# Performance work log

Measured on AMD Instinct MI355X. Metric: run time of the kernel, lower is better.

Reference implementation:

```python
import jax, jax.numpy as jnp
import numpy as np

# Module configuration (from init_kwargs)
N, C_IN, C_OUT, L, V, P = 4, 64, 64, 1024, 25, 3
KERNEL_SIZE, STRIDE = 9, 1
EPS = 1e-5


def _toeplitz(length):
    # Faithful to: sum_i pad(eye(L - stride*i), (i*stride, 0, 0, i*stride))
    # -> ones at [r, r + i*stride] for i in range(kernel_size // stride)
    t = jnp.zeros((length, length), dtype=jnp.float32)
    for i in range(KERNEL_SIZE // STRIDE):  # small fixed loop over taps
        t = t + jnp.eye(length, k=i * STRIDE, dtype=jnp.float32)
    return t


def setup_inputs() -> dict:
    key = jax.random.key(0)
    k0, k1, k2, k3 = jax.random.split(key, 4)
    x = jax.random.normal(k0, (N, C_IN, L, V), dtype=jnp.float32)
    A = jax.random.uniform(k1, (P, V, V), dtype=jnp.float32)
    edge_importance = jnp.ones((P, V, V), dtype=jnp.float32)
    conv_w = jax.random.normal(k2, (C_OUT * P, C_IN, 1, 1), dtype=jnp.float32) * 0.05
    conv_b = jax.random.normal(k3, (C_OUT * P,), dtype=jnp.float32) * 0.05
    gamma = jnp.ones((C_OUT,), dtype=jnp.float32)
    beta = jnp.zeros((C_OUT,), dtype=jnp.float32)
    return {"x": x, "A": A, "edge_importance": edge_importance,
            "conv_w": conv_w, "conv_b": conv_b, "gamma": gamma, "beta": beta}


def reference(x, A, edge_importance, conv_w, conv_b, gamma, beta):
    n, _, l, v = x.shape
    res = x  # residual: in_channels == out_channels and stride == 1 -> identity

    # 1x1 conv: (N, C_in, L, V) -> (N, P*C_out, L, V)
    w = conv_w[:, :, 0, 0]  # (P*C_out, C_in)
    y = jnp.einsum('nclv,kc->nklv', x, w) + conv_b[None, :, None, None]

    # split into P chunks of C_out along channels, stack, permute -> (N, L, P, C_out, V)
    y = y.reshape(n, P, C_OUT, l, v).transpose(0, 3, 1, 2, 4)

    # partition-wise graph adjacency matmul with edge-importance mask
    y = jnp.einsum('nlpcv,pvw->nlpcw', y, A * edge_importance)

    # Toeplitz temporal conv: (N, P, C, V, L) @ (L, L)
    y = y.transpose(0, 2, 3, 4, 1)
    y = jnp.matmul(y, _toeplitz(l))
    y = y.sum(axis=1)            # sum over partitions -> (N, C, V, L)
    y = y.transpose(0, 1, 3, 2)  # (N, C, L, V)

    # BatchNorm2d with batch statistics (track_running_stats=False) + ReLU
    mean = y.mean(axis=(0, 2, 3), keepdims=True)
    var = y.var(axis=(0, 2, 3), keepdims=True)  # biased, as torch uses for normalization
    y = (y - mean) * jax.lax.rsqrt(var + EPS)
    y = y * gamma[None, :, None, None] + beta[None, :, None, None]
    y = jax.nn.relu(y)

    # do = Sequential(ReLU, Dropout(0.0)) applied to (y + res)
    return jax.nn.relu(y + res)
```

## Files before the change

### kernel.cpp

```cpp
#include <hip/hip_runtime.h>


typedef unsigned short ushort_t;
typedef __attribute__((ext_vector_type(8))) short short8;
typedef __attribute__((ext_vector_type(4))) float f32x4;
typedef __attribute__((ext_vector_type(4))) unsigned short us4;
typedef __attribute__((ext_vector_type(8))) unsigned short us8;

#define N_  4
#define CI_ 64
#define CO_ 64
#define L_  1024
#define V_  25
#define P_  3
#define KS_ 9
#define NLV 102400.0f
#define NREP 128

__device__ __forceinline__ float b2f(ushort_t u) {
  union { float f; unsigned int i; } c; c.i = ((unsigned int)u) << 16; return c.f;
}
__device__ __forceinline__ ushort_t f2b(float f) {
  union { float f; unsigned int i; } c; c.f = f;
  unsigned int u = c.i;
  u += 0x7fffu + ((u >> 16) & 1u);
  return (ushort_t)(u >> 16);
}

__global__ __launch_bounds__(256) void kwin(
    const float* __restrict__ x, ushort_t* __restrict__ xs,
    const float* __restrict__ A, const float* __restrict__ E,
    const float* __restrict__ cb, const float* __restrict__ W,
    ushort_t* __restrict__ a2raw, float* __restrict__ biastab,
    ushort_t* __restrict__ wb, float* __restrict__ statsbuf)
{
  const int chunk = blockIdx.x;
  const int n = blockIdx.y;
  const int tid = threadIdx.x;

  if (chunk == 128) {
    if (n != 0) return;
    __shared__ float colA[P_ * 32];
    if (tid < P_ * 32) {
      int p = tid >> 5, w = tid & 31;
      float s = 0.f;
      if (w < V_)
        for (int v = 0; v < V_; ++v) {
          int idx = (p * V_ + v) * V_ + w;
          s += A[idx] * E[idx];
        }
      colA[tid] = s;
    }
    for (int e = tid; e < 32 * 96; e += 256) {
      int w = e / 96, k = e - w * 96;
      int p = k >> 5, v = k & 31;
      float val = 0.f;
      if (w < V_ && v < V_) {
        int idx = (p * V_ + v) * V_ + w;
        val = A[idx] * E[idx];
      }
      a2raw[e] = f2b(val);
    }
    for (int e = tid; e < 192 * 64; e += 256) wb[e] = f2b(W[e]);
    __syncthreads();
    for (int e = tid; e < 32 * 64; e += 256) {
      int w = e >> 6, c = e & 63;
      float s = 0.f;
      for (int p = 0; p < P_; ++p) s += cb[p * 64 + c] * colA[p * 32 + w];
      biastab[e] = s;
    }
    for (int e = tid; e < NREP * 128; e += 256) statsbuf[e] = 0.f;
    return;
  }

  __shared__ ushort_t tile[64 * 402];
  const int l0 = chunk * 8;
  const long xn = (long)n * CI_ * L_ * V_;
  for (int m = tid; m < 6400; m += 256) {
    int ci = m / 100;
    int j4 = (m - ci * 100) * 4;
    f32x4 d;
    if (chunk == 0 && j4 < 200) {
      d = (f32x4){0.f, 0.f, 0.f, 0.f};
    } else {
      d = *(const f32x4*)(x + xn + (long)ci * (L_ * V_) + (l0 - 8) * V_ + j4);
    }
    ushort_t* dst = &tile[ci * 402 + j4];
    dst[0] = f2b(d[0]); dst[1] = f2b(d[1]); dst[2] = f2b(d[2]); dst[3] = f2b(d[3]);
  }
  __syncthreads();
  const long xsbase = ((long)n * L_ + l0) * 1600;
  for (int cid = tid; cid < 1600; cid += 256) {
    const int v = cid >> 6, ci = cid & 63;
    const ushort_t* col = &tile[ci * 402 + v];
    float s = 0.f;
#pragma unroll
    for (int li = 0; li < 9; ++li) s += b2f(col[li * 25]);
    xs[xsbase + cid] = f2b(s);
#pragma unroll
    for (int l_ = 1; l_ < 8; ++l_) {
      s += b2f(col[(l_ + 8) * 25]) - b2f(col[(l_ - 1) * 25]);
      xs[xsbase + l_ * 1600 + cid] = f2b(s);
    }
  }
}

__global__ __launch_bounds__(256, 4) void kmain(
    const ushort_t* __restrict__ xs,
    const ushort_t* __restrict__ Wb,
    const ushort_t* __restrict__ a2,
    const float*    __restrict__ biastab,
    ushort_t*       __restrict__ zb,
    float*          __restrict__ statsbuf)
{
  const int lb = blockIdx.x;
  const int n  = blockIdx.y;
  const int tid = threadIdx.x, lane = tid & 63, wv = tid >> 6;
  const int m16 = lane & 15, quad = lane >> 4;

  __shared__ __align__(16) ushort_t T1[13312];

  short8 af[3][2];
#pragma unroll
  for (int i = 0; i < 3; ++i) {
    const ushort_t* wrow = Wb + ((wv * 3 + i) * 16 + m16) * 64 + quad * 8;
    af[i][0] = *(const short8*)(wrow);
    af[i][1] = *(const short8*)(wrow + 32);
  }

  const ushort_t* xsb = xs + ((long)n * L_ + 4 * lb) * 1600;
  const int cbase = wv * 16 + quad * 4;
  float s1[4] = {0.f, 0.f, 0.f, 0.f}, s2[4] = {0.f, 0.f, 0.f, 0.f};

#pragma unroll
  for (int pair = 0; pair < 2; ++pair) {
    short8 bfr[4][2];
#pragma unroll
    for (int nt = 0; nt < 4; ++nt) {
      const int v = (nt & 1) * 16 + m16;
      const int l_ = pair * 2 + (nt >> 1);
#pragma unroll
      for (int ks = 0; ks < 2; ++ks) {
        short8 t = (short8){0, 0, 0, 0, 0, 0, 0, 0};
        if (v < V_)
          t = *(const short8*)(xsb + l_ * 1600 + v * 64 + ks * 32 + quad * 8);
        bfr[nt][ks] = t;
      }
    }

    f32x4 acc1[3][4];
#pragma unroll
    for (int i = 0; i < 3; ++i)
#pragma unroll
      for (int j = 0; j < 4; ++j) acc1[i][j] = (f32x4){0.f, 0.f, 0.f, 0.f};

#pragma unroll
    for (int i = 0; i < 3; ++i)
#pragma unroll
      for (int nt = 0; nt < 4; ++nt) {
        acc1[i][nt] = __builtin_amdgcn_mfma_f32_16x16x32_bf16(af[i][0], bfr[nt][0], acc1[i][nt], 0, 0, 0);
        acc1[i][nt] = __builtin_amdgcn_mfma_f32_16x16x32_bf16(af[i][1], bfr[nt][1], acc1[i][nt], 0, 0, 0);
      }

    if (pair) __syncthreads();
#pragma unroll
    for (int i = 0; i < 3; ++i) {
      const int mt = wv * 3 + i;
#pragma unroll
      for (int nt = 0; nt < 4; ++nt) {
        const int l_ = nt >> 1;
        const int col = (nt & 1) * 16 + m16;
#pragma unroll
        for (int r = 0; r < 4; ++r) {
          int k = mt * 16 + quad * 4 + r;
          T1[l_ * 6656 + (k & 63) * 104 + (k >> 6) * 32 + col] = f2b(acc1[i][nt][r]);
        }
      }
    }
    __syncthreads();

    short8 bfr2[2][3];
#pragma unroll
    for (int nt = 0; nt < 2; ++nt)
#pragma unroll
      for (int ks = 0; ks < 3; ++ks)
        bfr2[nt][ks] = *(const short8*)(a2 + (nt * 16 + m16) * 96 + ks * 32 + quad * 8);

    f32x4 acc2[2][2];
#pragma unroll
    for (int l_ = 0; l_ < 2; ++l_)
#pragma unroll
      for (int nt = 0; nt < 2; ++nt) acc2[l_][nt] = (f32x4){0.f, 0.f, 0.f, 0.f};

#pragma unroll
    for (int l_ = 0; l_ < 2; ++l_)
#pragma unroll
      for (int ks = 0; ks < 3; ++ks) {
        short8 afT = *(const short8*)(&T1[l_ * 6656 + (wv * 16 + m16) * 104 + ks * 32 + quad * 8]);
        acc2[l_][0] = __builtin_amdgcn_mfma_f32_16x16x32_bf16(afT, bfr2[0][ks], acc2[l_][0], 0, 0, 0);
        acc2[l_][1] = __builtin_amdgcn_mfma_f32_16x16x32_bf16(afT, bfr2[1][ks], acc2[l_][1], 0, 0, 0);
      }

#pragma unroll
    for (int l_ = 0; l_ < 2; ++l_) {
      const int l = 4 * lb + pair * 2 + l_;
      const float cnt = (float)(l + 1 < KS_ ? l + 1 : KS_);
#pragma unroll
      for (int nt = 0; nt < 2; ++nt) {
        const int w = nt * 16 + m16;
        if (w < V_) {
          f32x4 bias = *(const f32x4*)(biastab + w * 64 + cbase);
          us4 pack;
#pragma unroll
          for (int r = 0; r < 4; ++r) {
            pack[r] = f2b(acc2[l_][nt][r] + cnt * bias[r]);
            float zr = b2f(pack[r]);
            s1[r] += zr; s2[r] += zr * zr;
          }
          *(us4*)(&zb[(((long)(n * L_ + l) * V_ + w) << 6) + cbase]) = pack;
        }
      }
    }
  }
#pragma unroll
  for (int off = 1; off < 16; off <<= 1) {
#pragma unroll
    for (int r = 0; r < 4; ++r) {
      s1[r] += __shfl_xor(s1[r], off, 64);
      s2[r] += __shfl_xor(s2[r], off, 64);
    }
  }
  if (m16 == 0) {
    float* sb = statsbuf + ((n * 256 + lb) & (NREP - 1)) * 128;
#pragma unroll
    for (int r = 0; r < 4; ++r) {
      atomicAdd(&sb[cbase + r], s1[r]);
      atomicAdd(&sb[64 + cbase + r], s2[r]);
    }
  }
}

__global__ __launch_bounds__(256) void kapply(
    const ushort_t* __restrict__ zb, const float* __restrict__ x,
    const float* __restrict__ statsbuf,
    const float* __restrict__ gamma, const float* __restrict__ beta,
    float* __restrict__ out)
{
  const int n = blockIdx.y, chunk = blockIdx.x;
  const int tid = threadIdx.x;
  __shared__ ushort_t zl[200 * 66];
  __shared__ float red[4][64][2];
  __shared__ float sc[64], sh[64];
  const long zbase = (long)((n * L_ + chunk * 8) * V_) * 64;
  for (int m = tid; m < 6400; m += 256) {
    *(unsigned int*)(&zl[(m >> 5) * 66 + (m & 31) * 2]) =
        ((const unsigned int*)(zb + zbase))[m];
  }
  {
    const int c = tid & 63, grp = tid >> 6;
    float a = 0.f, b = 0.f;
    for (int k = grp; k < NREP; k += 4) {
      a += statsbuf[k * 128 + c];
      b += statsbuf[k * 128 + 64 + c];
    }
    red[grp][c][0] = a;
    red[grp][c][1] = b;
  }
  __syncthreads();
  if (tid < 64) {
    const float inv = 1.0f / NLV;
    float s  = red[0][tid][0] + red[1][tid][0] + red[2][tid][0] + red[3][tid][0];
    float sq = red[0][tid][1] + red[1][tid][1] + red[2][tid][1] + red[3][tid][1];
    float mean = s * inv;
    float var  = sq * inv - mean * mean;
    float rstd = rsqrtf(var + 1e-5f);
    float g = gamma[tid];
    sc[tid] = rstd * g;
    sh[tid] = beta[tid] - mean * rstd * g;
  }
  __syncthreads();
  const long obase = ((long)(n * 64) * L_ + chunk * 8) * V_;
  for (int m = tid; m < 3200; m += 256) {
    int c = m / 50, q = m - c * 50, rr = q * 4;
    long xi = obase + (long)c * (L_ * V_) + rr;
    f32x4 xv = *(const f32x4*)(x + xi);
    f32x4 o;
#pragma unroll
    for (int j = 0; j < 4; ++j) {
      float z = b2f(zl[(rr + j) * 66 + c]);
      float y = fmaxf(z * sc[c] + sh[c], 0.f);
      o[j] = fmaxf(y + xv[j], 0.f);
    }
    *(f32x4*)(out + xi) = o;
  }
}

extern "C" void kernel_launch(void* const* d_in, const int* in_sizes, int n_in,
                              void* d_out, int out_size, void* d_ws, size_t ws_size,
                              hipStream_t stream)
{
  const float* x     = (const float*)d_in[0];
  const float* A     = (const float*)d_in[1];
  const float* E     = (const float*)d_in[2];
  const float* W     = (const float*)d_in[3];
  const float* cb    = (const float*)d_in[4];
  const float* gamma = (const float*)d_in[5];
  const float* beta  = (const float*)d_in[6];
  float* out = (float*)d_out;

  char* ws = (char*)d_ws;
  const size_t XS_OFF   = 0;
  const size_t ZB_OFF   = 13107200;
  const size_t WB_OFF   = 26214400;
  const size_t A2_OFF   = WB_OFF + 32768;
  const size_t BIAS_OFF = A2_OFF + 16384;
  const size_t STAT_OFF = BIAS_OFF + 16384;
  ushort_t* xs       = (ushort_t*)(ws + XS_OFF);
  ushort_t* zb       = (ushort_t*)(ws + ZB_OFF);
  ushort_t* wb       = (ushort_t*)(ws + WB_OFF);
  ushort_t* a2       = (ushort_t*)(ws + A2_OFF);
  float*    biastab  = (float*)(ws + BIAS_OFF);
  float*    statsbuf = (float*)(ws + STAT_OFF);

  kwin  <<<dim3(129, N_), 256, 0, stream>>>(x, xs, A, E, cb, W, a2, biastab, wb,
                                            statsbuf);
  kmain <<<dim3(256, N_), 256, 0, stream>>>(xs, wb, a2, biastab, zb, statsbuf);
  kapply<<<dim3(128, N_), 256, 0, stream>>>(zb, x, statsbuf, gamma, beta, out);
}
```

Measured before the change: 135.1 us.

## Pack LDS writes, hoist kmain loads, swizzle apply tile, vectorize stats reduce

Several independent changes across three kernels. In kwin the bf16 tile writes are packed into 32-bit stores with a padded stride, and each thread now handles two channels so its xs stores are 32-bit. In kmain all xs B-fragment loads for both pairs are issued up front, and the MFMA accumulators are reduced to one row-tile at a time. In kapply the LDS transpose tile uses an XOR swizzle to cut bank conflicts, and the stats reduction reads float4. These trade extra register pressure in kmain for more overlap of load latency.

```diff
diff --git a/kernel.cpp b/kernel.cpp
--- a/kernel.cpp
+++ b/kernel.cpp
@@ -5,7 +5,6 @@
 typedef __attribute__((ext_vector_type(8))) short short8;
 typedef __attribute__((ext_vector_type(4))) float f32x4;
 typedef __attribute__((ext_vector_type(4))) unsigned short us4;
-typedef __attribute__((ext_vector_type(8))) unsigned short us8;
 
 #define N_  4
 #define CI_ 64
@@ -16,6 +15,7 @@
 #define KS_ 9
 #define NLV 102400.0f
 #define NREP 128
+#define TSTR 406
 
 __device__ __forceinline__ float b2f(ushort_t u) {
   union { float f; unsigned int i; } c; c.i = ((unsigned int)u) << 16; return c.f;
@@ -73,7 +73,7 @@
     return;
   }
 
-  __shared__ ushort_t tile[64 * 402];
+  __shared__ __align__(16) ushort_t tile[64 * TSTR];
   const int l0 = chunk * 8;
   const long xn = (long)n * CI_ * L_ * V_;
   for (int m = tid; m < 6400; m += 256) {
@@ -85,22 +85,28 @@
     } else {
       d = *(const f32x4*)(x + xn + (long)ci * (L_ * V_) + (l0 - 8) * V_ + j4);
     }
-    ushort_t* dst = &tile[ci * 402 + j4];
-    dst[0] = f2b(d[0]); dst[1] = f2b(d[1]); dst[2] = f2b(d[2]); dst[3] = f2b(d[3]);
+    unsigned int p0 = (unsigned int)f2b(d[0]) | ((unsigned int)f2b(d[1]) << 16);
+    unsigned int p1 = (unsigned int)f2b(d[2]) | ((unsigned int)f2b(d[3]) << 16);
+    *(unsigned int*)(&tile[ci * TSTR + j4])     = p0;
+    *(unsigned int*)(&tile[ci * TSTR + j4 + 2]) = p1;
   }
   __syncthreads();
   const long xsbase = ((long)n * L_ + l0) * 1600;
-  for (int cid = tid; cid < 1600; cid += 256) {
-    const int v = cid >> 6, ci = cid & 63;
-    const ushort_t* col = &tile[ci * 402 + v];
-    float s = 0.f;
-#pragma unroll
-    for (int li = 0; li < 9; ++li) s += b2f(col[li * 25]);
-    xs[xsbase + cid] = f2b(s);
+  for (int cp = tid; cp < 800; cp += 256) {
+    const int v = cp >> 5, ci = (cp & 31) * 2;
+    const ushort_t* c0 = &tile[ci * TSTR + v];
+    const ushort_t* c1 = c0 + TSTR;
+    float s0 = 0.f, s1 = 0.f;
+#pragma unroll
+    for (int li = 0; li < 9; ++li) { s0 += b2f(c0[li * 25]); s1 += b2f(c1[li * 25]); }
+    *(unsigned int*)(xs + xsbase + v * 64 + ci) =
+        (unsigned int)f2b(s0) | ((unsigned int)f2b(s1) << 16);
 #pragma unroll
     for (int l_ = 1; l_ < 8; ++l_) {
-      s += b2f(col[(l_ + 8) * 25]) - b2f(col[(l_ - 1) * 25]);
-      xs[xsbase + l_ * 1600 + cid] = f2b(s);
+      s0 += b2f(c0[(l_ + 8) * 25]) - b2f(c0[(l_ - 1) * 25]);
+      s1 += b2f(c1[(l_ + 8) * 25]) - b2f(c1[(l_ - 1) * 25]);
+      *(unsigned int*)(xs + xsbase + l_ * 1600 + v * 64 + ci) =
+          (unsigned int)f2b(s0) | ((unsigned int)f2b(s1) << 16);
     }
   }
 }
@@ -120,6 +126,24 @@
 
   __shared__ __align__(16) ushort_t T1[13312];
 
+  const ushort_t* xsb = xs + ((long)n * L_ + 4 * lb) * 1600;
+
+  short8 bfr[2][4][2];
+#pragma unroll
+  for (int pair = 0; pair < 2; ++pair)
+#pragma unroll
+    for (int nt = 0; nt < 4; ++nt) {
+      const int v = (nt & 1) * 16 + m16;
+      const int l_ = pair * 2 + (nt >> 1);
+#pragma unroll
+      for (int ks = 0; ks < 2; ++ks) {
+        short8 t = (short8){0, 0, 0, 0, 0, 0, 0, 0};
+        if (v < V_)
+          t = *(const short8*)(xsb + l_ * 1600 + v * 64 + ks * 32 + quad * 8);
+        bfr[pair][nt][ks] = t;
+      }
+    }
+
   short8 af[3][2];
 #pragma unroll
   for (int i = 0; i < 3; ++i) {
@@ -128,43 +152,23 @@
     af[i][1] = *(const short8*)(wrow + 32);
   }
 
-  const ushort_t* xsb = xs + ((long)n * L_ + 4 * lb) * 1600;
   const int cbase = wv * 16 + quad * 4;
   float s1[4] = {0.f, 0.f, 0.f, 0.f}, s2[4] = {0.f, 0.f, 0.f, 0.f};
 
 #pragma unroll
   for (int pair = 0; pair < 2; ++pair) {
-    short8 bfr[4][2];
-#pragma unroll
-    for (int nt = 0; nt < 4; ++nt) {
-      const int v = (nt & 1) * 16 + m16;
-      const int l_ = pair * 2 + (nt >> 1);
-#pragma unroll
-      for (int ks = 0; ks < 2; ++ks) {
-        short8 t = (short8){0, 0, 0, 0, 0, 0, 0, 0};
-        if (v < V_)
-          t = *(const short8*)(xsb + l_ * 1600 + v * 64 + ks * 32 + quad * 8);
-        bfr[nt][ks] = t;
-      }
-    }
-
-    f32x4 acc1[3][4];
-#pragma unroll
-    for (int i = 0; i < 3; ++i)
-#pragma unroll
-      for (int j = 0; j < 4; ++j) acc1[i][j] = (f32x4){0.f, 0.f, 0.f, 0.f};
-
-#pragma unroll
-    for (int i = 0; i < 3; ++i)
+    if (pair) __syncthreads();
+
+#pragma unroll
+    for (int i = 0; i < 3; ++i) {
+      f32x4 acc[4];
+#pragma unroll
+      for (int nt = 0; nt < 4; ++nt) acc[nt] = (f32x4){0.f, 0.f, 0.f, 0.f};
 #pragma unroll
       for (int nt = 0; nt < 4; ++nt) {
-        acc1[i][nt] = __builtin_amdgcn_mfma_f32_16x16x32_bf16(af[i][0], bfr[nt][0], acc1[i][nt], 0, 0, 0);
-        acc1[i][nt] = __builtin_amdgcn_mfma_f32_16x16x32_bf16(af[i][1], bfr[nt][1], acc1[i][nt], 0, 0, 0);
-      }
-
-    if (pair) __syncthreads();
-#pragma unroll
-    for (int i = 0; i < 3; ++i) {
+        acc[nt] = __builtin_amdgcn_mfma_f32_16x16x32_bf16(af[i][0], bfr[pair][nt][0], acc[nt], 0, 0, 0);
+        acc[nt] = __builtin_amdgcn_mfma_f32_16x16x32_bf16(af[i][1], bfr[pair][nt][1], acc[nt], 0, 0, 0);
+      }
       const int mt = wv * 3 + i;
 #pragma unroll
       for (int nt = 0; nt < 4; ++nt) {
@@ -173,7 +177,7 @@
 #pragma unroll
         for (int r = 0; r < 4; ++r) {
           int k = mt * 16 + quad * 4 + r;
-          T1[l_ * 6656 + (k & 63) * 104 + (k >> 6) * 32 + col] = f2b(acc1[i][nt][r]);
+          T1[l_ * 6656 + (k & 63) * 104 + (k >> 6) * 32 + col] = f2b(acc[nt][r]);
         }
       }
     }
@@ -248,29 +252,34 @@
 {
   const int n = blockIdx.y, chunk = blockIdx.x;
   const int tid = threadIdx.x;
-  __shared__ ushort_t zl[200 * 66];
-  __shared__ float red[4][64][2];
+  __shared__ __align__(16) ushort_t zl[200 * 66];
+  __shared__ f32x4 red[8][32];
   __shared__ float sc[64], sh[64];
   const long zbase = (long)((n * L_ + chunk * 8) * V_) * 64;
   for (int m = tid; m < 6400; m += 256) {
-    *(unsigned int*)(&zl[(m >> 5) * 66 + (m & 31) * 2]) =
-        ((const unsigned int*)(zb + zbase))[m];
+    const int row = m >> 5, c2 = (m & 31) * 2;
+    const int cs = c2 ^ (((row >> 2) & 31) << 1);
+    *(unsigned int*)(&zl[row * 66 + cs]) = ((const unsigned int*)(zb + zbase))[m];
   }
   {
-    const int c = tid & 63, grp = tid >> 6;
-    float a = 0.f, b = 0.f;
-    for (int k = grp; k < NREP; k += 4) {
-      a += statsbuf[k * 128 + c];
-      b += statsbuf[k * 128 + 64 + c];
-    }
-    red[grp][c][0] = a;
-    red[grp][c][1] = b;
+    const int s4 = tid & 31, grp = tid >> 5;
+    const f32x4* sb4 = (const f32x4*)statsbuf;
+    f32x4 a = (f32x4){0.f, 0.f, 0.f, 0.f};
+    for (int k = grp; k < NREP; k += 8) {
+      f32x4 v = sb4[k * 32 + s4];
+      a[0] += v[0]; a[1] += v[1]; a[2] += v[2]; a[3] += v[3];
+    }
+    red[grp][s4] = a;
   }
   __syncthreads();
   if (tid < 64) {
     const float inv = 1.0f / NLV;
-    float s  = red[0][tid][0] + red[1][tid][0] + red[2][tid][0] + red[3][tid][0];
-    float sq = red[0][tid][1] + red[1][tid][1] + red[2][tid][1] + red[3][tid][1];
+    float s = 0.f, sq = 0.f;
+#pragma unroll
+    for (int g = 0; g < 8; ++g) {
+      s  += red[g][tid >> 2][tid & 3];
+      sq += red[g][16 + (tid >> 2)][tid & 3];
+    }
     float mean = s * inv;
     float var  = sq * inv - mean * mean;
     float rstd = rsqrtf(var + 1e-5f);
@@ -282,13 +291,15 @@
   const long obase = ((long)(n * 64) * L_ + chunk * 8) * V_;
   for (int m = tid; m < 3200; m += 256) {
     int c = m / 50, q = m - c * 50, rr = q * 4;
+    const int e = ((q & 31) << 1);
     long xi = obase + (long)c * (L_ * V_) + rr;
     f32x4 xv = *(const f32x4*)(x + xi);
+    const float scc = sc[c], shc = sh[c];
     f32x4 o;
 #pragma unroll
     for (int j = 0; j < 4; ++j) {
-      float z = b2f(zl[(rr + j) * 66 + c]);
-      float y = fmaxf(z * sc[c] + sh[c], 0.f);
+      float z = b2f(zl[(rr + j) * 66 + (c ^ e)]);
+      float y = fmaxf(z * scc + shc, 0.f);
       o[j] = fmaxf(y + xv[j], 0.f);
     }
     *(f32x4*)(out + xi) = o;
```

Measured after the change: 138.7 us. 1.03x slower.
